# Performance work log

Hardware: AMD Instinct MI355X
Metric: run time of the kernel (lower is better)

Reference implementation:

```python
import jax, jax.numpy as jnp
import numpy as np

HIDDEN = 768
HEADS = 12
HEAD_DIM = HIDDEN // HEADS
ORDER = 5


def setup_inputs() -> dict:
    key = jax.random.key(0)
    ks = jax.random.split(key, 8)
    s = 0.02
    return {
        "hidden_states": jax.random.normal(ks[0], (4, 2048, HIDDEN), jnp.float32),
        "Wq": jax.random.normal(ks[1], (HIDDEN, HIDDEN), jnp.float32) * s,
        "bq": jnp.zeros((HIDDEN,), jnp.float32),
        "Wk": jax.random.normal(ks[2], (HIDDEN, HIDDEN), jnp.float32) * s,
        "bk": jnp.zeros((HIDDEN,), jnp.float32),
        "Wv": jax.random.normal(ks[3], (HIDDEN, HIDDEN), jnp.float32) * s,
        "bv": jnp.zeros((HIDDEN,), jnp.float32),
        "alphas": jax.random.normal(ks[4], (HEADS, ORDER + 1), jnp.float32) * s,
    }


def _chebyshev_bias(alphas, seq_len, dtype):
    pos = jnp.arange(seq_len, dtype=dtype)
    # rel[i, j] = j - i, normalized to [-1, 1]
    denom = dtype.type(max(seq_len - 1, 1)) if hasattr(dtype, 'type') else float(max(seq_len - 1, 1))
    x = jnp.clip((pos[None, :] - pos[:, None]) / float(max(seq_len - 1, 1)), -1.0, 1.0)
    t0 = jnp.ones_like(x)
    polys = [t0, x]
    for _ in range(2, ORDER + 1):
        polys.append(2.0 * x * polys[-1] - polys[-2])
    tk = jnp.stack(polys, axis=-1)  # [S, S, order+1]
    return jnp.einsum('hk,ijk->hij', alphas, tk)  # [H, S, S]


def reference(hidden_states, Wq, bq, Wk, bk, Wv, bv, alphas):
    b, s, _ = hidden_states.shape

    def split_heads(t):
        return t.reshape(b, s, HEADS, HEAD_DIM).transpose(0, 2, 1, 3)

    q = split_heads(hidden_states @ Wq.T + bq)  # [B, H, S, D]
    k = split_heads(hidden_states @ Wk.T + bk)
    v = split_heads(hidden_states @ Wv.T + bv)

    scores = jnp.einsum('bhid,bhjd->bhij', q, k) / jnp.sqrt(
        jnp.asarray(HEAD_DIM, hidden_states.dtype))
    scores = scores + _chebyshev_bias(alphas, s, hidden_states.dtype)[None]
    probs = jax.nn.softmax(scores, axis=-1)
    ctx = jnp.einsum('bhij,bhjd->bhid', probs, v)  # [B, H, S, D]
    return ctx.transpose(0, 2, 1, 3).reshape(b, s, HIDDEN)
```

## Files before the change

### kernel.cpp

```cpp
#include <hip/hip_runtime.h>
#include <hip/hip_fp16.h>

#define HIDDEN 768
#define HEADS 12
#define HDIM 64
#define SEQ 2048
#define BATCH 4
#define ORDER 5
#define LOG2E 1.44269504088896f

typedef _Float16 f16;
typedef _Float16 f16x8 __attribute__((ext_vector_type(8)));
typedef _Float16 f16x4 __attribute__((ext_vector_type(4)));
typedef float f32x4 __attribute__((ext_vector_type(4)));

#define MFMA16x16x32(A, B, C) __builtin_amdgcn_mfma_f32_16x16x32_f16(A, B, C, 0, 0, 0)

#define GLD16(gptr, lptr)                                                     \
    __builtin_amdgcn_global_load_lds(                                         \
        (const __attribute__((address_space(1))) void*)(gptr),                \
        (__attribute__((address_space(3))) void*)(lptr), 16, 0, 0)

#define NXG (8192 * 768 / 8)
#define NWG (768 * 768 / 8)
#define NCVT (NXG + 3 * NWG)
#define NBIAS (HEADS * (2 * SEQ - 1))

__global__ __launch_bounds__(256)
void prep_kernel(const float* __restrict__ X,
                 const float* __restrict__ Wq, const float* __restrict__ Wk,
                 const float* __restrict__ Wv, const float* __restrict__ alphas,
                 f16* __restrict__ Xh, f16* __restrict__ Wh,
                 float* __restrict__ biasTab)
{
    const int tid = blockIdx.x * 256 + threadIdx.x;
    if (tid < NCVT) {
        const float* src;
        f16* dst;
        size_t off;
        if (tid < NXG)               { src = X;  dst = Xh;              off = (size_t)tid * 8; }
        else if (tid < NXG + NWG)    { src = Wq; dst = Wh;              off = (size_t)(tid - NXG) * 8; }
        else if (tid < NXG + 2*NWG)  { src = Wk; dst = Wh + 768 * 768;  off = (size_t)(tid - NXG - NWG) * 8; }
        else                         { src = Wv; dst = Wh + 2*768*768;  off = (size_t)(tid - NXG - 2*NWG) * 8; }
        float4 a = *(const float4*)(src + off);
        float4 b = *(const float4*)(src + off + 4);
        f16x8 h;
        h[0] = (f16)a.x; h[1] = (f16)a.y; h[2] = (f16)a.z; h[3] = (f16)a.w;
        h[4] = (f16)b.x; h[5] = (f16)b.y; h[6] = (f16)b.z; h[7] = (f16)b.w;
        *(f16x8*)(dst + off) = h;
    } else {
        int idx = tid - NCVT;
        if (idx >= NBIAS) return;
        const int W = 2 * SEQ - 1;
        int h = idx / W;
        int t = idx - h * W;
        float x = (float)(t - (SEQ - 1)) / (float)(SEQ - 1);
        float tp = 1.0f;
        float tc = x;
        float acc = alphas[h * (ORDER + 1) + 0] * tp + alphas[h * (ORDER + 1) + 1] * tc;
#pragma unroll
        for (int k = 2; k <= ORDER; ++k) {
            float tn = 2.0f * x * tc - tp;
            acc += alphas[h * (ORDER + 1) + k] * tn;
            tp = tc; tc = tn;
        }
        biasTab[idx] = acc * LOG2E;
    }
}

__global__ __launch_bounds__(256)
void qkv_kernel(const f16* __restrict__ Xh, const f16* __restrict__ Wh,
                const float* __restrict__ bq, const float* __restrict__ bk,
                const float* __restrict__ bv,
                f16* __restrict__ qf, f16* __restrict__ kf, f16* __restrict__ vtf)
{
    const int wgid = (blockIdx.x & 7) * 144 + (blockIdx.x >> 3);
    const int tileM = wgid / 18;
    const int tileN = wgid % 18;
    const int m0 = tileM * 128;
    const int n0g = tileN * 128;
    const int w = tileN / 6;
    const int nloc0 = n0g - w * 768;
    const float* __restrict__ bias = (w == 0) ? bq : (w == 1) ? bk : bv;

    __shared__ __align__(16) f16 sA[128][32];
    __shared__ __align__(16) f16 sB[128][32];

    const int t = threadIdx.x;
    const int lane = t & 63;
    const int wv = t >> 6;
    const int wm = wv >> 1, wn = wv & 1;
    const int fr = lane & 15;
    const int kg = lane >> 4;

    const int srow = lane >> 2;
    const int scol = (lane & 3) * 8;

    f32x4 acc[4][4];
#pragma unroll
    for (int i = 0; i < 4; ++i)
#pragma unroll
        for (int j = 0; j < 4; ++j) acc[i][j] = (f32x4)(0.0f);

    const f16* gA = Xh + (size_t)(m0 + wv * 32 + srow) * 768 + scol;
    const f16* gB = Wh + (size_t)(n0g + wv * 32 + srow) * 768 + scol;
    f16* lA0 = &sA[wv * 32][0];
    f16* lA1 = &sA[wv * 32 + 16][0];
    f16* lB0 = &sB[wv * 32][0];
    f16* lB1 = &sB[wv * 32 + 16][0];

    for (int kt = 0; kt < 768; kt += 32) {
        __syncthreads();
        GLD16(gA + kt, lA0);
        GLD16(gA + kt + 16 * 768, lA1);
        GLD16(gB + kt, lB0);
        GLD16(gB + kt + 16 * 768, lB1);
        __syncthreads();

        f16x8 af[4], bf[4];
#pragma unroll
        for (int i = 0; i < 4; ++i) {
            af[i] = *(const f16x8*)&sA[wm * 64 + i * 16 + fr][kg * 8];
            bf[i] = *(const f16x8*)&sB[wn * 64 + i * 16 + fr][kg * 8];
        }
#pragma unroll
        for (int mi = 0; mi < 4; ++mi)
#pragma unroll
            for (int ni = 0; ni < 4; ++ni)
                acc[mi][ni] = MFMA16x16x32(af[mi], bf[ni], acc[mi][ni]);
    }

    const int bb = m0 >> 11;
#pragma unroll
    for (int mi = 0; mi < 4; ++mi) {
        const int s0 = (m0 & 2047) + wm * 64 + mi * 16 + kg * 4;
#pragma unroll
        for (int ni = 0; ni < 4; ++ni) {
            const int nloc = nloc0 + wn * 64 + ni * 16 + fr;
            const int hh = nloc >> 6, d = nloc & 63;
            const size_t bh = (size_t)bb * HEADS + hh;
            const float bc = bias[nloc];
            if (w == 2) {
                f16x4 pv;
#pragma unroll
                for (int r = 0; r < 4; ++r) pv[r] = (f16)(acc[mi][ni][r] + bc);
                *(f16x4*)&vtf[(bh * HDIM + d) * SEQ + s0] = pv;
            } else if (w == 0) {
#pragma unroll
                for (int r = 0; r < 4; ++r)
                    qf[(bh * SEQ + s0 + r) * HDIM + d] =
                        (f16)((acc[mi][ni][r] + bc) * (0.125f * LOG2E));
            } else {
#pragma unroll
                for (int r = 0; r < 4; ++r)
                    kf[(bh * SEQ + s0 + r) * HDIM + d] = (f16)(acc[mi][ni][r] + bc);
            }
        }
    }
}

struct __align__(16) SMem {
    union {
        struct {
            f16 sK[64][64];
            f16 sVT[64][64];
        } kv;
        float sO[4][16][72];
    } u;
    f16 sP[4][32][64];
};

__global__ __launch_bounds__(256, 3)
void attn_kernel(const f16* __restrict__ qf, const f16* __restrict__ kf,
                 const f16* __restrict__ vtf, const float* __restrict__ biasTab,
                 float* __restrict__ out)
{
    const int xcd = blockIdx.x & 7;
    const int ii = blockIdx.x >> 3;
    const int qt = ii & 15;
    const int bh = (ii >> 4) * 8 + xcd;
    const int h = bh % HEADS;
    const int b = bh / HEADS;
    const int q0 = qt * 128;

    __shared__ SMem sm;

    const int t = threadIdx.x;
    const int lane = t & 63;
    const int wv = t >> 6;
    const int fr = lane & 15;
    const int kg = lane >> 4;
    const int r7 = fr & 7;

    const int ubl = kg * 4 - wv * 32 - fr + 127;
    const float* const gB = biasTab + (size_t)h * (2 * SEQ - 1) + 1920 - q0 + ubl;

    f16x8 aq[2][2];
#pragma unroll
    for (int s = 0; s < 2; ++s)
#pragma unroll
        for (int c = 0; c < 2; ++c)
            aq[s][c] = *(const f16x8*)(qf +
                ((size_t)bh * SEQ + q0 + wv * 32 + s * 16 + fr) * HDIM + c * 32 + kg * 8);

    f32x4 oacc[2][4];
    float lsum[2] = {0.0f, 0.0f};
#pragma unroll
    for (int s = 0; s < 2; ++s)
#pragma unroll
        for (int df = 0; df < 4; ++df) oacc[s][df] = (f32x4)(0.0f);

    const int srow = t >> 2;
    const int scol = (t & 3) * 16;
    const int sw0 = 8 * (((t & 3) * 2) ^ (srow & 7));
    const int sw1 = 8 * (((t & 3) * 2 + 1) ^ (srow & 7));
    const f16* const gkb = kf + ((size_t)bh * SEQ + srow) * HDIM + scol;
    const f16* const gvb = vtf + ((size_t)bh * HDIM + srow) * SEQ + scol;
    f16* const myP = &sm.sP[wv][0][0];

    f16x8 rk0, rk1, rv0, rv1;
    auto stage_load = [&](int j0) {
        rk0 = *(const f16x8*)(gkb + (size_t)j0 * HDIM);
        rk1 = *(const f16x8*)(gkb + (size_t)j0 * HDIM + 8);
        rv0 = *(const f16x8*)(gvb + j0);
        rv1 = *(const f16x8*)(gvb + j0 + 8);
    };
    auto stage_write = [&]() {
        *(f16x8*)&sm.u.kv.sK[srow][sw0]  = rk0;
        *(f16x8*)&sm.u.kv.sK[srow][sw1]  = rk1;
        *(f16x8*)&sm.u.kv.sVT[srow][sw0] = rv0;
        *(f16x8*)&sm.u.kv.sVT[srow][sw1] = rv1;
    };

    float rb[5][4];
    auto bias_load = [&](int j0, float (&dst)[5][4]) {
#pragma unroll
        for (int g = 0; g < 5; ++g)
#pragma unroll
            for (int r = 0; r < 4; ++r)
                dst[g][r] = gB[j0 + (g - 1) * 16 + r];
    };

    stage_load(0);
    bias_load(0, rb);
    stage_write();
    __syncthreads();

    for (int j0 = 0; j0 < SEQ; j0 += 64) {
        const bool more = (j0 + 64 < SEQ);
        float rbn[5][4];
        if (more) {
            stage_load(j0 + 64);
            bias_load(j0 + 64, rbn);
        }

        f32x4 tt[2][4];
#pragma unroll
        for (int s = 0; s < 2; ++s)
#pragma unroll
            for (int ni = 0; ni < 4; ++ni)
#pragma unroll
                for (int r = 0; r < 4; ++r) tt[s][ni][r] = rb[ni - s + 1][r];

        __builtin_amdgcn_s_setprio(1);
#pragma unroll
        for (int ni = 0; ni < 4; ++ni) {
            const f16* kb = &sm.u.kv.sK[ni * 16 + fr][0];
            f16x8 bk0 = *(const f16x8*)(kb + 8 * (kg ^ r7));
            f16x8 bk1 = *(const f16x8*)(kb + 8 * ((kg + 4) ^ r7));
            tt[0][ni] = MFMA16x16x32(bk0, aq[0][0], tt[0][ni]);
            tt[0][ni] = MFMA16x16x32(bk1, aq[0][1], tt[0][ni]);
            tt[1][ni] = MFMA16x16x32(bk0, aq[1][0], tt[1][ni]);
            tt[1][ni] = MFMA16x16x32(bk1, aq[1][1], tt[1][ni]);
        }
        __builtin_amdgcn_s_setprio(0);

#pragma unroll
        for (int s = 0; s < 2; ++s) {
            float ls = 0.0f;
#pragma unroll
            for (int ni = 0; ni < 4; ++ni) {
                f16x4 ph;
#pragma unroll
                for (int r = 0; r < 4; ++r) {
                    float p = __builtin_amdgcn_exp2f(tt[s][ni][r]);
                    ls += p;
                    ph[r] = (f16)p;
                }
                *(f16x4*)(myP + (s * 16 + fr) * 64 +
                          (((ni * 2 + (kg >> 1)) ^ r7) * 8) + (kg & 1) * 4) = ph;
            }
            lsum[s] += ls;
        }

        f16x8 ap00 = *(const f16x8*)(myP + fr * 64 + 8 * (kg ^ r7));
        f16x8 ap01 = *(const f16x8*)(myP + fr * 64 + 8 * ((kg + 4) ^ r7));
        f16x8 ap10 = *(const f16x8*)(myP + (16 + fr) * 64 + 8 * (kg ^ r7));
        f16x8 ap11 = *(const f16x8*)(myP + (16 + fr) * 64 + 8 * ((kg + 4) ^ r7));
        __builtin_amdgcn_s_setprio(1);
#pragma unroll
        for (int df = 0; df < 4; ++df) {
            const f16* vb = &sm.u.kv.sVT[df * 16 + fr][0];
            f16x8 bv0 = *(const f16x8*)(vb + 8 * (kg ^ r7));
            f16x8 bv1 = *(const f16x8*)(vb + 8 * ((kg + 4) ^ r7));
            oacc[0][df] = MFMA16x16x32(bv0, ap00, oacc[0][df]);
            oacc[0][df] = MFMA16x16x32(bv1, ap01, oacc[0][df]);
            oacc[1][df] = MFMA16x16x32(bv0, ap10, oacc[1][df]);
            oacc[1][df] = MFMA16x16x32(bv1, ap11, oacc[1][df]);
        }
        __builtin_amdgcn_s_setprio(0);

        __syncthreads();
        if (more) {
            stage_write();
#pragma unroll
            for (int g = 0; g < 5; ++g)
#pragma unroll
                for (int r = 0; r < 4; ++r) rb[g][r] = rbn[g][r];
            __syncthreads();
        }
    }

    float inv[2];
#pragma unroll
    for (int s = 0; s < 2; ++s) {
        float l = lsum[s];
        l += __shfl_xor(l, 16, 64);
        l += __shfl_xor(l, 32, 64);
        inv[s] = 1.0f / l;
    }

    __syncthreads();
#pragma unroll
    for (int s = 0; s < 2; ++s) {
#pragma unroll
        for (int df = 0; df < 4; ++df) {
            f32x4 v = oacc[s][df];
            v *= inv[s];
            *(f32x4*)&sm.u.sO[wv][fr][df * 16 + kg * 4] = v;
        }
        int row = lane >> 2;
        int cb = (lane & 3) * 16;
        float* dst = out + ((size_t)b * SEQ + q0 + wv * 32 + s * 16 + row) * HIDDEN
                         + h * HDIM + cb;
#pragma unroll
        for (int i = 0; i < 4; ++i) {
            f32x4 v = *(const f32x4*)&sm.u.sO[wv][row][cb + 4 * i];
            *(f32x4*)(dst + 4 * i) = v;
        }
    }
}

extern "C" void kernel_launch(void* const* d_in, const int* in_sizes, int n_in,
                              void* d_out, int out_size, void* d_ws, size_t ws_size,
                              hipStream_t stream) {
    const float* X      = (const float*)d_in[0];
    const float* Wq     = (const float*)d_in[1];
    const float* bq     = (const float*)d_in[2];
    const float* Wk     = (const float*)d_in[3];
    const float* bk     = (const float*)d_in[4];
    const float* Wv     = (const float*)d_in[5];
    const float* bv     = (const float*)d_in[6];
    const float* alphas = (const float*)d_in[7];
    float* out = (float*)d_out;

    const size_t nQ = (size_t)BATCH * HEADS * SEQ * HDIM;
    f16* qf  = (f16*)d_ws;
    f16* kf  = qf + nQ;
    f16* vtf = kf + nQ;
    float* biasTab = (float*)(vtf + nQ);
    f16* Xh = (f16*)(biasTab + 49152);
    f16* Wh = Xh + (size_t)8192 * 768;

    const int prep_threads = NCVT + NBIAS;
    hipLaunchKernelGGL(prep_kernel, dim3((prep_threads + 255) / 256), dim3(256), 0,
                       stream, X, Wq, Wk, Wv, alphas, Xh, Wh, biasTab);
    hipLaunchKernelGGL(qkv_kernel, dim3(1152), dim3(256), 0, stream,
                       Xh, Wh, bq, bk, bv, qf, kf, vtf);
    hipLaunchKernelGGL(attn_kernel, dim3(BATCH * HEADS * 16), dim3(256), 0, stream,
                       qf, kf, vtf, biasTab, out);
}
```

Before: 134.5 us.

## Keep softmax probabilities in registers by permuting V^T sequence layout

The P tile no longer round-trips through shared memory. Probabilities are packed straight from the QK^T MFMA output registers into the PV MFMA operands with cvt_pkrtz. To make that register layout match, the projection kernel now writes V^T with a permuted sequence order inside each 32-key group, so the PV MFMA reduction lines up. This removes the LDS writes and reads of P and shrinks shared memory, which may help occupancy. In exchange, fp16 conversion now rounds toward zero, and correctness depends on the permutation exactly matching the MFMA lane mapping.

```diff
diff --git a/kernel.cpp b/kernel.cpp
--- a/kernel.cpp
+++ b/kernel.cpp
@@ -12,6 +12,7 @@
 typedef _Float16 f16;
 typedef _Float16 f16x8 __attribute__((ext_vector_type(8)));
 typedef _Float16 f16x4 __attribute__((ext_vector_type(4)));
+typedef __fp16 fp16x2 __attribute__((ext_vector_type(2)));
 typedef float f32x4 __attribute__((ext_vector_type(4)));
 
 #define MFMA16x16x32(A, B, C) __builtin_amdgcn_mfma_f32_16x16x32_f16(A, B, C, 0, 0, 0)
@@ -134,6 +135,8 @@
 #pragma unroll
     for (int mi = 0; mi < 4; ++mi) {
         const int s0 = (m0 & 2047) + wm * 64 + mi * 16 + kg * 4;
+        const int u = s0 & 31;
+        const int s0p = (s0 & ~31) | (((u >> 2) & 3) << 3) | (((u >> 4) & 1) << 2);
 #pragma unroll
         for (int ni = 0; ni < 4; ++ni) {
             const int nloc = nloc0 + wn * 64 + ni * 16 + fr;
@@ -144,7 +147,7 @@
                 f16x4 pv;
 #pragma unroll
                 for (int r = 0; r < 4; ++r) pv[r] = (f16)(acc[mi][ni][r] + bc);
-                *(f16x4*)&vtf[(bh * HDIM + d) * SEQ + s0] = pv;
+                *(f16x4*)&vtf[(bh * HDIM + d) * SEQ + s0p] = pv;
             } else if (w == 0) {
 #pragma unroll
                 for (int r = 0; r < 4; ++r)
@@ -167,7 +170,6 @@
         } kv;
         float sO[4][16][72];
     } u;
-    f16 sP[4][32][64];
 };
 
 __global__ __launch_bounds__(256, 3)
@@ -216,7 +218,6 @@
     const int sw1 = 8 * (((t & 3) * 2 + 1) ^ (srow & 7));
     const f16* const gkb = kf + ((size_t)bh * SEQ + srow) * HDIM + scol;
     const f16* const gvb = vtf + ((size_t)bh * HDIM + srow) * SEQ + scol;
-    f16* const myP = &sm.sP[wv][0][0];
 
     f16x8 rk0, rk1, rv0, rv1;
     auto stage_load = [&](int j0) {
@@ -275,38 +276,42 @@
         }
         __builtin_amdgcn_s_setprio(0);
 
+        union { fp16x2 h2[4]; f16x8 v8; } ap[2][2];
 #pragma unroll
         for (int s = 0; s < 2; ++s) {
             float ls = 0.0f;
-#pragma unroll
-            for (int ni = 0; ni < 4; ++ni) {
-                f16x4 ph;
+            float pv[4][4];
+#pragma unroll
+            for (int ni = 0; ni < 4; ++ni)
 #pragma unroll
                 for (int r = 0; r < 4; ++r) {
                     float p = __builtin_amdgcn_exp2f(tt[s][ni][r]);
+                    pv[ni][r] = p;
                     ls += p;
-                    ph[r] = (f16)p;
                 }
-                *(f16x4*)(myP + (s * 16 + fr) * 64 +
-                          (((ni * 2 + (kg >> 1)) ^ r7) * 8) + (kg & 1) * 4) = ph;
-            }
+#pragma unroll
+            for (int m = 0; m < 2; ++m)
+#pragma unroll
+                for (int nr = 0; nr < 2; ++nr) {
+                    const int ni = 2 * m + nr;
+                    ap[s][m].h2[nr * 2 + 0] =
+                        __builtin_amdgcn_cvt_pkrtz(pv[ni][0], pv[ni][1]);
+                    ap[s][m].h2[nr * 2 + 1] =
+                        __builtin_amdgcn_cvt_pkrtz(pv[ni][2], pv[ni][3]);
+                }
             lsum[s] += ls;
         }
 
-        f16x8 ap00 = *(const f16x8*)(myP + fr * 64 + 8 * (kg ^ r7));
-        f16x8 ap01 = *(const f16x8*)(myP + fr * 64 + 8 * ((kg + 4) ^ r7));
-        f16x8 ap10 = *(const f16x8*)(myP + (16 + fr) * 64 + 8 * (kg ^ r7));
-        f16x8 ap11 = *(const f16x8*)(myP + (16 + fr) * 64 + 8 * ((kg + 4) ^ r7));
         __builtin_amdgcn_s_setprio(1);
 #pragma unroll
         for (int df = 0; df < 4; ++df) {
             const f16* vb = &sm.u.kv.sVT[df * 16 + fr][0];
             f16x8 bv0 = *(const f16x8*)(vb + 8 * (kg ^ r7));
             f16x8 bv1 = *(const f16x8*)(vb + 8 * ((kg + 4) ^ r7));
-            oacc[0][df] = MFMA16x16x32(bv0, ap00, oacc[0][df]);
-            oacc[0][df] = MFMA16x16x32(bv1, ap01, oacc[0][df]);
-            oacc[1][df] = MFMA16x16x32(bv0, ap10, oacc[1][df]);
-            oacc[1][df] = MFMA16x16x32(bv1, ap11, oacc[1][df]);
+            oacc[0][df] = MFMA16x16x32(bv0, ap[0][0].v8, oacc[0][df]);
+            oacc[0][df] = MFMA16x16x32(bv1, ap[0][1].v8, oacc[0][df]);
+            oacc[1][df] = MFMA16x16x32(bv0, ap[1][0].v8, oacc[1][df]);
+            oacc[1][df] = MFMA16x16x32(bv1, ap[1][1].v8, oacc[1][df]);
         }
         __builtin_amdgcn_s_setprio(0);
 
```

After: 127.2 us (median of 2 runs). 1.06x faster.
